# Kernel tuning notes

Hardware: AMD Instinct MI355X
Metric: run time of the kernel (lower is better)

Reference implementation:

```python
import jax, jax.numpy as jnp
import numpy as np

B, N = 64, 1024

def setup_inputs() -> dict:
    key = jax.random.key(0)
    k1, k2 = jax.random.split(key)
    real = jax.random.normal(k1, (B, N), dtype=jnp.float32)
    imag = jax.random.normal(k2, (B, N), dtype=jnp.float32)
    return {"real": real, "imag": imag}

def reference(real, imag):
    # Batched complex outer product psi psi^dagger, split into real/imag parts.
    # real part:  r r^T + i i^T   ; imag part: -r i^T + i r^T
    r_col = real[:, :, None]   # [B, N, 1]
    r_row = real[:, None, :]   # [B, 1, N]
    i_col = imag[:, :, None]
    i_row = imag[:, None, :]
    out_rr = r_col * r_row + i_col * i_row          # [B, N, N]
    out_ii = -r_col * i_row + i_col * r_row          # [B, N, N]
    return (out_rr, out_ii)
```

## Files before the change

kernel.cpp:

```cpp
#include <hip/hip_runtime.h>


typedef float f32x4 __attribute__((ext_vector_type(4)));

constexpr int B_ = 64;
constexpr int N_ = 1024;
constexpr int ROWS = 8;

__global__ __launch_bounds__(256) void qouter_kernel(
    const float* __restrict__ real,
    const float* __restrict__ imag,
    float* __restrict__ out) {
    const int blk = blockIdx.x;
    const int b   = blk >> 7;
    const int i0  = (blk & 127) * ROWS;
    const int t   = threadIdx.x;

    const float* rrow = real + (size_t)b * N_;
    const float* irow = imag + (size_t)b * N_;

    const f32x4 rj = reinterpret_cast<const f32x4*>(rrow)[t];
    const f32x4 ij = reinterpret_cast<const f32x4*>(irow)[t];

    f32x4* out4    = reinterpret_cast<f32x4*>(out);
    size_t f4_rr   = ((size_t)b * N_ + i0) * (N_ / 4) + t;
    const size_t f4_off_ii = (size_t)B_ * N_ * (N_ / 4);

#pragma unroll
    for (int r = 0; r < ROWS; ++r) {
        const float rc = rrow[i0 + r];
        const float ic = irow[i0 + r];

        f32x4 orr = rc * rj + ic * ij;
        f32x4 oii = ic * rj - rc * ij;

        __builtin_nontemporal_store(orr, out4 + f4_rr);
        __builtin_nontemporal_store(oii, out4 + f4_rr + f4_off_ii);
        f4_rr += N_ / 4;
    }
}

extern "C" void kernel_launch(void* const* d_in, const int* in_sizes, int n_in,
                              void* d_out, int out_size, void* d_ws, size_t ws_size,
                              hipStream_t stream) {
    const float* real = (const float*)d_in[0];
    const float* imag = (const float*)d_in[1];
    float* out = (float*)d_out;

    dim3 grid(B_ * (N_ / ROWS));
    dim3 block(256);
    qouter_kernel<<<grid, block, 0, stream>>>(real, imag, out);
}
```

Baseline: 102.6 us.

## Use persistent grid-stride kernel writing output in fully linear order

```diff
diff --git a/kernel.cpp b/kernel.cpp
--- a/kernel.cpp
+++ b/kernel.cpp
@@ -5,38 +5,42 @@
 
 constexpr int B_ = 64;
 constexpr int N_ = 1024;
-constexpr int ROWS = 8;
+constexpr int NBLK = 2048;
+constexpr int NTHR = 256;
+constexpr size_t TOTAL_F4   = (size_t)2 * B_ * N_ * N_ / 4;
+constexpr size_t GRID_THREADS = (size_t)NBLK * NTHR;
+constexpr int    ITERS      = (int)(TOTAL_F4 / GRID_THREADS);
+constexpr size_t HALF_F4    = TOTAL_F4 / 2;
 
-__global__ __launch_bounds__(256) void qouter_kernel(
+__global__ __launch_bounds__(NTHR) void qouter_kernel(
     const float* __restrict__ real,
     const float* __restrict__ imag,
     float* __restrict__ out) {
-    const int blk = blockIdx.x;
-    const int b   = blk >> 7;
-    const int i0  = (blk & 127) * ROWS;
-    const int t   = threadIdx.x;
+    const size_t gid = (size_t)blockIdx.x * NTHR + threadIdx.x;
 
-    const float* rrow = real + (size_t)b * N_;
-    const float* irow = imag + (size_t)b * N_;
+    const int b0 = (int)(gid >> 18);
+    const int i  = (int)((gid & 262143) >> 8);
+    const int j4 = (int)(gid & 255);
 
-    const f32x4 rj = reinterpret_cast<const f32x4*>(rrow)[t];
-    const f32x4 ij = reinterpret_cast<const f32x4*>(irow)[t];
+    f32x4* out4 = reinterpret_cast<f32x4*>(out);
 
-    f32x4* out4    = reinterpret_cast<f32x4*>(out);
-    size_t f4_rr   = ((size_t)b * N_ + i0) * (N_ / 4) + t;
-    const size_t f4_off_ii = (size_t)B_ * N_ * (N_ / 4);
+#pragma unroll 4
+    for (int k = 0; k < ITERS; ++k) {
+        const int  b    = b0 + 2 * (k & 31);
+        const bool iiH  = (k >= 32);
+        const size_t f  = gid + (size_t)k * GRID_THREADS;
 
-#pragma unroll
-    for (int r = 0; r < ROWS; ++r) {
-        const float rc = rrow[i0 + r];
-        const float ic = irow[i0 + r];
+        const float* rrow = real + (size_t)b * N_;
+        const float* irow = imag + (size_t)b * N_;
+        const float rc = rrow[i];
+        const float ic = irow[i];
+        const f32x4 rj = reinterpret_cast<const f32x4*>(rrow)[j4];
+        const f32x4 ij = reinterpret_cast<const f32x4*>(irow)[j4];
 
-        f32x4 orr = rc * rj + ic * ij;
-        f32x4 oii = ic * rj - rc * ij;
-
-        __builtin_nontemporal_store(orr, out4 + f4_rr);
-        __builtin_nontemporal_store(oii, out4 + f4_rr + f4_off_ii);
-        f4_rr += N_ / 4;
+        f32x4 o;
+        if (!iiH) o = rc * rj + ic * ij;
+        else      o = ic * rj - rc * ij;
+        __builtin_nontemporal_store(o, out4 + f);
     }
 }
 
@@ -47,7 +51,5 @@
     const float* imag = (const float*)d_in[1];
     float* out = (float*)d_out;
 
-    dim3 grid(B_ * (N_ / ROWS));
-    dim3 block(256);
-    qouter_kernel<<<grid, block, 0, stream>>>(real, imag, out);
+    qouter_kernel<<<dim3(NBLK), dim3(NTHR), 0, stream>>>(real, imag, out);
 }
```

Result: slower. 119.2 us (+16.3%).
